# Optimization experiments

Hardware: AMD Instinct MI355X
Metric: run time of the kernel (lower is better)

## Reference

```python
import jax, jax.numpy as jnp
import numpy as np

# Static hypernetwork layer sizes from HyperOption(z_dim=256, inner_h=64, a_dim=32, layers=3)
SIZES = [256 * 64, 64, 64 * 64, 64, 64 * 32, 32]  # sum = 22688
SPLITS = np.cumsum(SIZES)[:-1]


def setup_inputs() -> dict:
    key = jax.random.key(0)
    ks = jax.random.split(key, 8)
    B, Z, H = 4096, 256, 1024
    return {
        "inputs": jax.random.normal(ks[0], (B, Z), dtype=jnp.float32),
        "option": jax.random.normal(ks[1], (B, sum(SIZES)), dtype=jnp.float32) * 0.05,
        "w1": jax.random.normal(ks[2], (H, Z), dtype=jnp.float32) * 0.05,
        "b1": jax.random.normal(ks[3], (H,), dtype=jnp.float32) * 0.05,
        "w2": jax.random.normal(ks[4], (H, H), dtype=jnp.float32) * 0.05,
        "b2": jax.random.normal(ks[5], (H,), dtype=jnp.float32) * 0.05,
        "w3": jax.random.normal(ks[6], (1, H), dtype=jnp.float32) * 0.05,
        "b3": jax.random.normal(ks[7], (1,), dtype=jnp.float32) * 0.05,
    }


def _apply_option(state, option):
    # Per-sample hypernetwork MLP: weights/biases packed in `option`.
    parts = jnp.split(option, SPLITS, axis=-1)
    cur = state
    n_layers = len(parts) // 2
    for i in range(n_layers):
        w = parts[2 * i].reshape(option.shape[0], -1, cur.shape[-1])  # [B, out, in]
        b = parts[2 * i + 1]                                          # [B, out]
        cur = jnp.einsum('boi,bi->bo', w, cur) + b
        if i < n_layers - 1:
            cur = jax.nn.relu(cur)
    return cur


def _value(z, w1, b1, w2, b2, w3, b3):
    t = jax.nn.elu(z @ w1.T + b1)
    t = jax.nn.elu(t @ w2.T + b2)
    return t @ w3.T + b3  # [B, 1]


def reference(inputs, option, w1, b1, w2, b2, w3, b3):
    value = _value(inputs, w1, b1, w2, b2, w3, b3)   # [B, 1]
    action = _apply_option(inputs, option)            # [B, 32]
    return jnp.concatenate([value, action], axis=-1)  # [B, 33]
```

## Files before the change

kernel.cpp:

```cpp
#include <hip/hip_runtime.h>
#include <hip/hip_bf16.h>
#include <cstdint>

typedef __attribute__((ext_vector_type(8))) short  short8;
typedef __attribute__((ext_vector_type(8))) __bf16 bf16x8;
typedef __attribute__((ext_vector_type(4))) float  floatx4;
typedef __attribute__((ext_vector_type(4))) float  f32x4;
typedef __attribute__((ext_vector_type(4))) short  short4v;

union Frag { short8 s; bf16x8 b; };

__device__ inline short f2bf(float f) {
    union { float f; unsigned u; } v; v.f = f;
    unsigned r = (v.u + 0x7fffu + ((v.u >> 16) & 1u)) >> 16;
    return (short)r;
}
__device__ inline float elu(float x) { return x > 0.f ? x : __expf(x) - 1.f; }

__device__ inline short8 load8_f32_to_bf16(const float* __restrict__ p) {
    float4 f0 = ((const float4*)p)[0];
    float4 f1 = ((const float4*)p)[1];
    short8 r;
    r[0] = f2bf(f0.x); r[1] = f2bf(f0.y); r[2] = f2bf(f0.z); r[3] = f2bf(f0.w);
    r[4] = f2bf(f1.x); r[5] = f2bf(f1.y); r[6] = f2bf(f1.z); r[7] = f2bf(f1.w);
    return r;
}
__device__ inline float dot4(f32x4 a, f32x4 b) {
    return a.x * b.x + a.y * b.y + a.z * b.z + a.w * b.w;
}
__device__ inline f32x4 ntload4(const f32x4* __restrict__ p) {
    return __builtin_nontemporal_load(p);
}
__device__ inline float ntload1(const float* __restrict__ p) {
    return __builtin_nontemporal_load(p);
}

#define B_SZ   4096
#define Z_DIM  256
#define H_DIM  1024
#define OUT_W  33
#define OFF_W1 0
#define OFF_B1 16384
#define OFF_W2 16448
#define OFF_B2 20544
#define OFF_W3 20608
#define OFF_B3 22656
#define OPT_W  22688

#define G1_BLOCKS 256
#define CONV_BLOCKS 64
#define G2_BLOCKS 512

template<int KTOT, int SM, int SN, bool ACONV, bool BCONV, bool VEPI>
__device__ __forceinline__ void gemm_tile(
    const void* __restrict__ Av, const void* __restrict__ Bv,
    const float* __restrict__ bias, const float* __restrict__ w3,
    __hip_bfloat16* __restrict__ T, float* __restrict__ out,
    int bm, int bn, int tid)
{
    const int lane = tid & 63, wid = tid >> 6;
    const int wm = wid >> 1, wn = wid & 1;
    const int m_wave = bm * (32 * SM) + wm * (16 * SM);
    const int n_wave = bn * (32 * SN) + wn * (16 * SN);
    const int lr = lane & 15, lk = (lane >> 4) * 8;

    floatx4 acc[SM][SN] = {};
    for (int k0 = 0; k0 < KTOT; k0 += 32) {
        Frag a[SM], bb[SN];
#pragma unroll
        for (int sm = 0; sm < SM; ++sm) {
            const size_t off = (size_t)(m_wave + sm * 16 + lr) * KTOT + k0 + lk;
            if constexpr (ACONV) a[sm].s = load8_f32_to_bf16((const float*)Av + off);
            else                 a[sm].s = *(const short8*)((const ushort*)Av + off);
        }
#pragma unroll
        for (int sn = 0; sn < SN; ++sn) {
            const size_t off = (size_t)(n_wave + sn * 16 + lr) * KTOT + k0 + lk;
            if constexpr (BCONV) bb[sn].s = load8_f32_to_bf16((const float*)Bv + off);
            else                 bb[sn].s = *(const short8*)((const ushort*)Bv + off);
        }
#pragma unroll
        for (int sm = 0; sm < SM; ++sm)
#pragma unroll
            for (int sn = 0; sn < SN; ++sn)
                acc[sm][sn] = __builtin_amdgcn_mfma_f32_16x16x32_bf16(
                    a[sm].b, bb[sn].b, acc[sm][sn], 0, 0, 0);
    }

    if constexpr (VEPI) {
        float bias_v[SN], w3_v[SN];
#pragma unroll
        for (int sn = 0; sn < SN; ++sn) {
            const int n = n_wave + sn * 16 + lr;
            bias_v[sn] = bias[n];
            w3_v[sn]   = w3[n];
        }
#pragma unroll
        for (int sm = 0; sm < SM; ++sm) {
#pragma unroll
            for (int r = 0; r < 4; ++r) {
                float rowsum = 0.f;
#pragma unroll
                for (int sn = 0; sn < SN; ++sn)
                    rowsum += elu(acc[sm][sn][r] + bias_v[sn]) * w3_v[sn];
                rowsum += __shfl_xor(rowsum, 1);
                rowsum += __shfl_xor(rowsum, 2);
                rowsum += __shfl_xor(rowsum, 4);
                rowsum += __shfl_xor(rowsum, 8);
                if (lr == 0) {
                    const int m = m_wave + sm * 16 + (lane >> 4) * 4 + r;
                    atomicAdd(out + (size_t)m * OUT_W, rowsum);
                }
            }
        }
    } else {
#pragma unroll
        for (int sm = 0; sm < SM; ++sm)
#pragma unroll
            for (int sn = 0; sn < SN; ++sn) {
                const int n = n_wave + sn * 16 + lr;
                const float bv = bias[n];
#pragma unroll
                for (int r = 0; r < 4; ++r) {
                    const int m = m_wave + sm * 16 + (lane >> 4) * 4 + r;
                    T[(size_t)m * H_DIM + n] = __float2bfloat16(elu(acc[sm][sn][r] + bv));
                }
            }
    }
}

__device__ __forceinline__ void hyper_sample(
    const float* __restrict__ z, const float* __restrict__ opt,
    float* __restrict__ out, int b, int tid,
    float* __restrict__ h1, float* __restrict__ h2)
{
    const int lane = tid & 63, w = tid >> 6;
    const int l16 = lane & 15, lg = lane >> 4;
    const float* __restrict__ orow = opt + (size_t)b * OPT_W;

    const f32x4* __restrict__ Z4 = (const f32x4*)(z + (size_t)b * Z_DIM);
    f32x4 zv[4];
#pragma unroll
    for (int p = 0; p < 4; ++p) zv[p] = Z4[p * 16 + l16];

    {
        const f32x4* __restrict__ W = (const f32x4*)(orow + OFF_W1) + (size_t)(w * 16) * 64;
        f32x4 wv[16];
#pragma unroll
        for (int g = 0; g < 4; ++g)
#pragma unroll
            for (int p = 0; p < 4; ++p)
                wv[g * 4 + p] = ntload4(W + (g * 4 + lg) * 64 + p * 16 + l16);
#pragma unroll
        for (int g = 0; g < 4; ++g) {
            float acc = 0.f;
#pragma unroll
            for (int p = 0; p < 4; ++p) acc += dot4(wv[g * 4 + p], zv[p]);
            acc += __shfl_xor(acc, 1);
            acc += __shfl_xor(acc, 2);
            acc += __shfl_xor(acc, 4);
            acc += __shfl_xor(acc, 8);
            const int r = 16 * w + g * 4 + lg;
            if (l16 == 0) h1[r] = fmaxf(acc + ntload1(orow + OFF_B1 + r), 0.f);
        }
    }
    __syncthreads();

    {
        const f32x4 h1v = *(const f32x4*)(h1 + 4 * l16);
        const f32x4* __restrict__ W = (const f32x4*)(orow + OFF_W2 + w * 16 * 64);
        f32x4 wv[4];
#pragma unroll
        for (int j = 0; j < 4; ++j) wv[j] = ntload4(W + j * 64 + lane);
#pragma unroll
        for (int j = 0; j < 4; ++j) {
            float p = dot4(wv[j], h1v);
            p += __shfl_xor(p, 1); p += __shfl_xor(p, 2);
            p += __shfl_xor(p, 4); p += __shfl_xor(p, 8);
            const int r = 16 * w + j * 4 + lg;
            if (l16 == 0) h2[r] = fmaxf(p + ntload1(orow + OFF_B2 + r), 0.f);
        }
    }
    __syncthreads();

    {
        const f32x4 h2v = *(const f32x4*)(h2 + 4 * l16);
        const f32x4* __restrict__ W = (const f32x4*)(orow + OFF_W3 + w * 8 * 64);
        f32x4 wv[2];
#pragma unroll
        for (int j = 0; j < 2; ++j) wv[j] = ntload4(W + j * 64 + lane);
#pragma unroll
        for (int j = 0; j < 2; ++j) {
            float p = dot4(wv[j], h2v);
            p += __shfl_xor(p, 1); p += __shfl_xor(p, 2);
            p += __shfl_xor(p, 4); p += __shfl_xor(p, 8);
            const int r = 8 * w + j * 4 + lg;
            if (l16 == 0) out[(size_t)b * OUT_W + 1 + r] = p + ntload1(orow + OFF_B3 + r);
        }
    }
}

__global__ __launch_bounds__(256) void kA_kernel(
    const float* __restrict__ z, const float* __restrict__ w1,
    const float* __restrict__ b1, const float* __restrict__ w2,
    const float* __restrict__ b3,
    __hip_bfloat16* __restrict__ T1, __hip_bfloat16* __restrict__ w2bf,
    float* __restrict__ out)
{
    const int blk = blockIdx.x, t = threadIdx.x;
    if (blk < G1_BLOCKS) {
        const int j = (blk & 7) * 32 + (blk >> 3);
        gemm_tile<Z_DIM, 4, 4, true, true, false>(z, w1, b1, nullptr, T1, nullptr,
                                                  j >> 3, j & 7, t);
    } else {
        const int gtid = (blk - G1_BLOCKS) * 256 + t;
        if (gtid < B_SZ) out[(size_t)gtid * OUT_W] = b3[0];
#pragma unroll
        for (int i = 0; i < 16; ++i) {
            const int v = gtid + i * 16384;
            float4 f = ((const float4*)w2)[v];
            short4v s;
            s[0] = f2bf(f.x); s[1] = f2bf(f.y); s[2] = f2bf(f.z); s[3] = f2bf(f.w);
            ((short4v*)w2bf)[v] = s;
        }
    }
}

__global__ __launch_bounds__(256) void kB_kernel(
    const float* __restrict__ z, const float* __restrict__ opt,
    float* __restrict__ out)
{
    __shared__ float h1[64], h2[64];
    hyper_sample(z, opt, out, blockIdx.x, threadIdx.x, h1, h2);
}

__global__ __launch_bounds__(256) void kC_kernel(
    const __hip_bfloat16* __restrict__ T1, const __hip_bfloat16* __restrict__ w2bf,
    const float* __restrict__ b2, const float* __restrict__ w3,
    float* __restrict__ out)
{
    const int blk = blockIdx.x, t = threadIdx.x;
    const int j = (blk & 7) * 64 + (blk >> 3);
    gemm_tile<H_DIM, 4, 2, false, false, true>(T1, w2bf, b2, w3, nullptr, out,
                                               j >> 4, j & 15, t);
}

extern "C" void kernel_launch(void* const* d_in, const int* in_sizes, int n_in,
                              void* d_out, int out_size, void* d_ws, size_t ws_size,
                              hipStream_t stream)
{
    const float* z   = (const float*)d_in[0];
    const float* opt = (const float*)d_in[1];
    const float* w1  = (const float*)d_in[2];
    const float* b1  = (const float*)d_in[3];
    const float* w2  = (const float*)d_in[4];
    const float* b2  = (const float*)d_in[5];
    const float* w3  = (const float*)d_in[6];
    const float* b3  = (const float*)d_in[7];
    float* out = (float*)d_out;

    __hip_bfloat16* T1   = (__hip_bfloat16*)d_ws;
    __hip_bfloat16* w2bf = (__hip_bfloat16*)((char*)d_ws +
                             (size_t)B_SZ * H_DIM * sizeof(__hip_bfloat16));

    kA_kernel<<<dim3(G1_BLOCKS + CONV_BLOCKS), dim3(256), 0, stream>>>(
        z, w1, b1, w2, b3, T1, w2bf, out);

    kB_kernel<<<dim3(B_SZ), dim3(256), 0, stream>>>(z, opt, out);

    kC_kernel<<<dim3(G2_BLOCKS), dim3(256), 0, stream>>>(T1, w2bf, b2, w3, out);
}
```

Before: 135.5 us.

## Split hypernetwork per layer and co-schedule with value GEMMs in two launches

The per-sample hypernetwork is split in two. Its first layer runs in the same launch as the first value GEMM and the w2 conversion, and writes h1 to workspace. Layers two and three run in the same launch as the second GEMM, whose tile shape changes from 4x2 to 4x4 subtiles (256 blocks instead of 512). This drops from three launches to two and lets the memory-bound option streaming overlap the compute-bound GEMMs. The cost is a global round trip for h1, plus larger GEMM tiles that may lower parallelism in the second GEMM.

```diff
diff --git a/kernel.cpp b/kernel.cpp
--- a/kernel.cpp
+++ b/kernel.cpp
@@ -47,9 +47,8 @@
 #define OFF_B3 22656
 #define OPT_W  22688
 
-#define G1_BLOCKS 256
+#define G_BLOCKS 256
 #define CONV_BLOCKS 64
-#define G2_BLOCKS 512
 
 template<int KTOT, int SM, int SN, bool ACONV, bool BCONV, bool VEPI>
 __device__ __forceinline__ void gemm_tile(
@@ -129,10 +128,9 @@
     }
 }
 
-__device__ __forceinline__ void hyper_sample(
+__device__ __forceinline__ void hyper_l1(
     const float* __restrict__ z, const float* __restrict__ opt,
-    float* __restrict__ out, int b, int tid,
-    float* __restrict__ h1, float* __restrict__ h2)
+    float* __restrict__ h1ws, int b, int tid)
 {
     const int lane = tid & 63, w = tid >> 6;
     const int l16 = lane & 15, lg = lane >> 4;
@@ -143,77 +141,84 @@
 #pragma unroll
     for (int p = 0; p < 4; ++p) zv[p] = Z4[p * 16 + l16];
 
-    {
-        const f32x4* __restrict__ W = (const f32x4*)(orow + OFF_W1) + (size_t)(w * 16) * 64;
-        f32x4 wv[16];
-#pragma unroll
-        for (int g = 0; g < 4; ++g)
-#pragma unroll
-            for (int p = 0; p < 4; ++p)
-                wv[g * 4 + p] = ntload4(W + (g * 4 + lg) * 64 + p * 16 + l16);
-#pragma unroll
-        for (int g = 0; g < 4; ++g) {
-            float acc = 0.f;
-#pragma unroll
-            for (int p = 0; p < 4; ++p) acc += dot4(wv[g * 4 + p], zv[p]);
-            acc += __shfl_xor(acc, 1);
-            acc += __shfl_xor(acc, 2);
-            acc += __shfl_xor(acc, 4);
-            acc += __shfl_xor(acc, 8);
-            const int r = 16 * w + g * 4 + lg;
-            if (l16 == 0) h1[r] = fmaxf(acc + ntload1(orow + OFF_B1 + r), 0.f);
-        }
+    const f32x4* __restrict__ W = (const f32x4*)(orow + OFF_W1) + (size_t)(w * 16) * 64;
+    f32x4 wv[16];
+#pragma unroll
+    for (int g = 0; g < 4; ++g)
+#pragma unroll
+        for (int p = 0; p < 4; ++p)
+            wv[g * 4 + p] = ntload4(W + (g * 4 + lg) * 64 + p * 16 + l16);
+
+#pragma unroll
+    for (int g = 0; g < 4; ++g) {
+        float acc = 0.f;
+#pragma unroll
+        for (int p = 0; p < 4; ++p) acc += dot4(wv[g * 4 + p], zv[p]);
+        acc += __shfl_xor(acc, 1);
+        acc += __shfl_xor(acc, 2);
+        acc += __shfl_xor(acc, 4);
+        acc += __shfl_xor(acc, 8);
+        const int r = 16 * w + g * 4 + lg;
+        if (l16 == 0)
+            h1ws[(size_t)b * 64 + r] = fmaxf(acc + ntload1(orow + OFF_B1 + r), 0.f);
+    }
+}
+
+__device__ __forceinline__ void hyper_l23(
+    const float* __restrict__ opt, const float* __restrict__ h1ws,
+    float* __restrict__ out, int b, int tid, float* __restrict__ h2)
+{
+    const int lane = tid & 63, w = tid >> 6;
+    const int l16 = lane & 15, lg = lane >> 4;
+    const float* __restrict__ orow = opt + (size_t)b * OPT_W;
+
+    const f32x4* __restrict__ W2 = (const f32x4*)(orow + OFF_W2) + (size_t)(w * 16) * 16;
+    f32x4 wv2[4];
+#pragma unroll
+    for (int j = 0; j < 4; ++j) wv2[j] = ntload4(W2 + j * 64 + lane);
+
+    const f32x4* __restrict__ W3 = (const f32x4*)(orow + OFF_W3) + (size_t)(w * 8) * 16;
+    f32x4 wv3[2];
+#pragma unroll
+    for (int j = 0; j < 2; ++j) wv3[j] = ntload4(W3 + j * 64 + lane);
+
+    const f32x4 h1v = *(const f32x4*)(h1ws + (size_t)b * 64 + 4 * l16);
+
+#pragma unroll
+    for (int j = 0; j < 4; ++j) {
+        float p = dot4(wv2[j], h1v);
+        p += __shfl_xor(p, 1); p += __shfl_xor(p, 2);
+        p += __shfl_xor(p, 4); p += __shfl_xor(p, 8);
+        const int r = 16 * w + j * 4 + lg;
+        if (l16 == 0) h2[r] = fmaxf(p + ntload1(orow + OFF_B2 + r), 0.f);
     }
     __syncthreads();
 
-    {
-        const f32x4 h1v = *(const f32x4*)(h1 + 4 * l16);
-        const f32x4* __restrict__ W = (const f32x4*)(orow + OFF_W2 + w * 16 * 64);
-        f32x4 wv[4];
-#pragma unroll
-        for (int j = 0; j < 4; ++j) wv[j] = ntload4(W + j * 64 + lane);
-#pragma unroll
-        for (int j = 0; j < 4; ++j) {
-            float p = dot4(wv[j], h1v);
-            p += __shfl_xor(p, 1); p += __shfl_xor(p, 2);
-            p += __shfl_xor(p, 4); p += __shfl_xor(p, 8);
-            const int r = 16 * w + j * 4 + lg;
-            if (l16 == 0) h2[r] = fmaxf(p + ntload1(orow + OFF_B2 + r), 0.f);
-        }
-    }
-    __syncthreads();
-
-    {
-        const f32x4 h2v = *(const f32x4*)(h2 + 4 * l16);
-        const f32x4* __restrict__ W = (const f32x4*)(orow + OFF_W3 + w * 8 * 64);
-        f32x4 wv[2];
-#pragma unroll
-        for (int j = 0; j < 2; ++j) wv[j] = ntload4(W + j * 64 + lane);
-#pragma unroll
-        for (int j = 0; j < 2; ++j) {
-            float p = dot4(wv[j], h2v);
-            p += __shfl_xor(p, 1); p += __shfl_xor(p, 2);
-            p += __shfl_xor(p, 4); p += __shfl_xor(p, 8);
-            const int r = 8 * w + j * 4 + lg;
-            if (l16 == 0) out[(size_t)b * OUT_W + 1 + r] = p + ntload1(orow + OFF_B3 + r);
-        }
-    }
-}
-
-__global__ __launch_bounds__(256) void kA_kernel(
-    const float* __restrict__ z, const float* __restrict__ w1,
-    const float* __restrict__ b1, const float* __restrict__ w2,
-    const float* __restrict__ b3,
+    const f32x4 h2v = *(const f32x4*)(h2 + 4 * l16);
+#pragma unroll
+    for (int j = 0; j < 2; ++j) {
+        float p = dot4(wv3[j], h2v);
+        p += __shfl_xor(p, 1); p += __shfl_xor(p, 2);
+        p += __shfl_xor(p, 4); p += __shfl_xor(p, 8);
+        const int r = 8 * w + j * 4 + lg;
+        if (l16 == 0) out[(size_t)b * OUT_W + 1 + r] = p + ntload1(orow + OFF_B3 + r);
+    }
+}
+
+__global__ __launch_bounds__(256) void h1_kernel(
+    const float* __restrict__ z, const float* __restrict__ opt,
+    const float* __restrict__ w1, const float* __restrict__ b1,
+    const float* __restrict__ w2, const float* __restrict__ b3,
     __hip_bfloat16* __restrict__ T1, __hip_bfloat16* __restrict__ w2bf,
-    float* __restrict__ out)
+    float* __restrict__ h1ws, float* __restrict__ out)
 {
     const int blk = blockIdx.x, t = threadIdx.x;
-    if (blk < G1_BLOCKS) {
+    if (blk < G_BLOCKS) {
         const int j = (blk & 7) * 32 + (blk >> 3);
         gemm_tile<Z_DIM, 4, 4, true, true, false>(z, w1, b1, nullptr, T1, nullptr,
                                                   j >> 3, j & 7, t);
-    } else {
-        const int gtid = (blk - G1_BLOCKS) * 256 + t;
+    } else if (blk < G_BLOCKS + CONV_BLOCKS) {
+        const int gtid = (blk - G_BLOCKS) * 256 + t;
         if (gtid < B_SZ) out[(size_t)gtid * OUT_W] = b3[0];
 #pragma unroll
         for (int i = 0; i < 16; ++i) {
@@ -223,26 +228,26 @@
             s[0] = f2bf(f.x); s[1] = f2bf(f.y); s[2] = f2bf(f.z); s[3] = f2bf(f.w);
             ((short4v*)w2bf)[v] = s;
         }
-    }
-}
-
-__global__ __launch_bounds__(256) void kB_kernel(
-    const float* __restrict__ z, const float* __restrict__ opt,
-    float* __restrict__ out)
-{
-    __shared__ float h1[64], h2[64];
-    hyper_sample(z, opt, out, blockIdx.x, threadIdx.x, h1, h2);
-}
-
-__global__ __launch_bounds__(256) void kC_kernel(
+    } else {
+        hyper_l1(z, opt, h1ws, blk - (G_BLOCKS + CONV_BLOCKS), t);
+    }
+}
+
+__global__ __launch_bounds__(256) void h23_kernel(
+    const float* __restrict__ opt, const float* __restrict__ h1ws,
     const __hip_bfloat16* __restrict__ T1, const __hip_bfloat16* __restrict__ w2bf,
     const float* __restrict__ b2, const float* __restrict__ w3,
     float* __restrict__ out)
 {
+    __shared__ float h2[64];
     const int blk = blockIdx.x, t = threadIdx.x;
-    const int j = (blk & 7) * 64 + (blk >> 3);
-    gemm_tile<H_DIM, 4, 2, false, false, true>(T1, w2bf, b2, w3, nullptr, out,
-                                               j >> 4, j & 15, t);
+    if (blk < G_BLOCKS) {
+        const int j = (blk & 7) * 32 + (blk >> 3);
+        gemm_tile<H_DIM, 4, 4, false, false, true>(T1, w2bf, b2, w3, nullptr, out,
+                                                   j >> 3, j & 7, t);
+    } else {
+        hyper_l23(opt, h1ws, out, blk - G_BLOCKS, t, h2);
+    }
 }
 
 extern "C" void kernel_launch(void* const* d_in, const int* in_sizes, int n_in,
@@ -260,13 +265,12 @@
     float* out = (float*)d_out;
 
     __hip_bfloat16* T1   = (__hip_bfloat16*)d_ws;
-    __hip_bfloat16* w2bf = (__hip_bfloat16*)((char*)d_ws +
-                             (size_t)B_SZ * H_DIM * sizeof(__hip_bfloat16));
-
-    kA_kernel<<<dim3(G1_BLOCKS + CONV_BLOCKS), dim3(256), 0, stream>>>(
-        z, w1, b1, w2, b3, T1, w2bf, out);
-
-    kB_kernel<<<dim3(B_SZ), dim3(256), 0, stream>>>(z, opt, out);
-
-    kC_kernel<<<dim3(G2_BLOCKS), dim3(256), 0, stream>>>(T1, w2bf, b2, w3, out);
-}
+    __hip_bfloat16* w2bf = (__hip_bfloat16*)((char*)d_ws + 8u * 1024 * 1024);
+    float*          h1ws = (float*)((char*)d_ws + 10u * 1024 * 1024);
+
+    h1_kernel<<<dim3(G_BLOCKS + CONV_BLOCKS + B_SZ), dim3(256), 0, stream>>>(
+        z, opt, w1, b1, w2, b3, T1, w2bf, h1ws, out);
+
+    h23_kernel<<<dim3(G_BLOCKS + B_SZ), dim3(256), 0, stream>>>(
+        opt, h1ws, T1, w2bf, b2, w3, out);
+}
```

After: 117.7 us. 1.15x faster.
